# Kernel tuning notes

Hardware: AMD Instinct MI355X
Metric: run time of the kernel (lower is better)

## Reference

```python
import jax, jax.numpy as jnp
import numpy as np
from jax import lax

H = 32  # hidden size (hardcoded in the torch module)

def setup_inputs() -> dict:
    key = jax.random.key(0)
    ks = jax.random.split(key, 7)
    B, T, I = 2048, 512, 64
    s = 1.0 / np.sqrt(H)  # torch nn.LSTM default init scale
    return {
        "x": jax.random.normal(ks[0], (B, T, I), dtype=jnp.float32),
        "W_ih": jax.random.uniform(ks[1], (4 * H, I), jnp.float32, -s, s),
        "W_hh": jax.random.uniform(ks[2], (4 * H, H), jnp.float32, -s, s),
        "b_ih": jax.random.uniform(ks[3], (4 * H,), jnp.float32, -s, s),
        "b_hh": jax.random.uniform(ks[4], (4 * H,), jnp.float32, -s, s),
        "W_fc": jax.random.uniform(ks[5], (1, H), jnp.float32, -s, s),
        "b_fc": jax.random.uniform(ks[6], (1,), jnp.float32, -s, s),
    }

def _lstm_last_h(x, W_ih, W_hh, b_ih, b_hh):
    B = x.shape[0]
    # Precompute input projections for all timesteps: [B, T, 4H] -> [T, B, 4H]
    xg = jnp.einsum('bti,gi->btg', x, W_ih) + (b_ih + b_hh)
    xg = jnp.transpose(xg, (1, 0, 2))

    def step(carry, xt):
        h, c = carry
        g = xt + h @ W_hh.T  # [B, 4H]
        i = jax.nn.sigmoid(g[:, 0 * H:1 * H])
        f = jax.nn.sigmoid(g[:, 1 * H:2 * H])
        gg = jnp.tanh(g[:, 2 * H:3 * H])
        o = jax.nn.sigmoid(g[:, 3 * H:4 * H])
        c = f * c + i * gg
        h = o * jnp.tanh(c)
        return (h, c), None

    init = (jnp.zeros((B, H), x.dtype), jnp.zeros((B, H), x.dtype))
    (h, _), _ = lax.scan(step, init, xg)
    return h  # [B, H], last timestep hidden state

def reference(x, W_ih, W_hh, b_ih, b_hh, W_fc, b_fc):
    # Dropout is identity in eval mode; only the last timestep feeds fc.
    h = _lstm_last_h(x, W_ih, W_hh, b_ih, b_hh)
    return h @ W_fc.T + b_fc  # [B, 1]
```

## Files before the change

kernel.cpp:

```cpp
#include <hip/hip_runtime.h>

typedef __attribute__((ext_vector_type(8))) short short8;
typedef __attribute__((ext_vector_type(4))) float f32x4;

#define LOG2E 1.44269504088896340736f

__device__ __forceinline__ unsigned short f2bf(float f) {
    union { float f; unsigned u; } a; a.f = f;
    unsigned r = a.u + 0x7fffu + ((a.u >> 16) & 1u);
    return (unsigned short)(r >> 16);
}
__device__ __forceinline__ unsigned pk2(float x, float y) {
    return (unsigned)f2bf(x) | ((unsigned)f2bf(y) << 16);
}
__device__ __forceinline__ float sigm(float x) {
    return __builtin_amdgcn_rcpf(1.0f + __builtin_amdgcn_exp2f(-LOG2E * x));
}

__global__ __launch_bounds__(256, 2) void lstm_fused(
    const float* __restrict__ x,
    const float* __restrict__ Wih,
    const float* __restrict__ Whh,
    const float* __restrict__ bih,
    const float* __restrict__ bhh,
    const float* __restrict__ Wfc,
    const float* __restrict__ bfc,
    float* __restrict__ out)
{
    __shared__ unsigned short Wlds[128 * 80];
    __shared__ float xg_sh[4 * 16 * 132];
    __shared__ alignas(64) unsigned short hbuf[4 * 32];

    const int tid  = threadIdx.x;
    const int lane = tid & 63;
    const int wv   = tid >> 6;
    const int b    = blockIdx.x * 4 + wv;
    const int m    = lane & 15;
    const int quad = lane >> 4;
    const int cc   = lane & 31;

    {
        const float4* w4 = (const float4*)Wih;
        unsigned* wl = (unsigned*)Wlds;
        #pragma unroll
        for (int i = 0; i < 8; i++) {
            int fi = tid * 8 + i;
            int g  = fi >> 4;
            int k  = (fi & 15) << 2;
            float4 v = w4[fi];
            wl[g * 40 + (k >> 1) + 0] = pk2(v.x, v.y);
            wl[g * 40 + (k >> 1) + 1] = pk2(v.z, v.w);
        }
    }

    short8 Bh[8];
    #pragma unroll
    for (int t = 0; t < 8; t++) {
        const float4* wr = (const float4*)(Whh + (size_t)(16 * t + m) * 32 + quad * 8);
        float4 va = wr[0], vb = wr[1];
        union { short8 v; unsigned u[4]; } B;
        B.u[0] = pk2(va.x, va.y); B.u[1] = pk2(va.z, va.w);
        B.u[2] = pk2(vb.x, vb.y); B.u[3] = pk2(vb.z, vb.w);
        Bh[t] = B.v;
    }

    float biasv[8];
    #pragma unroll
    for (int n = 0; n < 8; n++) biasv[n] = bih[16 * n + m] + bhh[16 * n + m];

    const bool b4 = (lane & 16) != 0;

    __syncthreads();

    const float* xrow = x + ((size_t)b * 512 + m) * 64;
    float* xgw = xg_sh + wv * 2112;
    unsigned short* hw = hbuf + wv * 32;

    hw[cc] = 0;
    float c = 0.0f, h = 0.0f;
    const f32x4 z4 = {0.f, 0.f, 0.f, 0.f};

    float4 p0, p1, p2, p3;
    {
        const float4* xr4 = (const float4*)xrow;
        p0 = xr4[quad * 2];     p1 = xr4[quad * 2 + 1];
        p2 = xr4[8 + quad * 2]; p3 = xr4[8 + quad * 2 + 1];
    }

    for (int ch = 0; ch < 32; ++ch) {
        union { short8 v; unsigned u[4]; } A0, A1;
        A0.u[0] = pk2(p0.x, p0.y); A0.u[1] = pk2(p0.z, p0.w);
        A0.u[2] = pk2(p1.x, p1.y); A0.u[3] = pk2(p1.z, p1.w);
        A1.u[0] = pk2(p2.x, p2.y); A1.u[1] = pk2(p2.z, p2.w);
        A1.u[2] = pk2(p3.x, p3.y); A1.u[3] = pk2(p3.z, p3.w);

        {
            const int chn = (ch < 31) ? ch + 1 : 31;
            const float4* nx = (const float4*)(xrow + (size_t)chn * 1024);
            p0 = nx[quad * 2];     p1 = nx[quad * 2 + 1];
            p2 = nx[8 + quad * 2]; p3 = nx[8 + quad * 2 + 1];
        }

        #pragma unroll
        for (int n = 0; n < 8; n++) {
            const short8 B0 = *(const short8*)&Wlds[(16 * n + m) * 80 + quad * 8];
            const short8 B1 = *(const short8*)&Wlds[(16 * n + m) * 80 + 32 + quad * 8];
            f32x4 acc = {0.f, 0.f, 0.f, 0.f};
            acc = __builtin_amdgcn_mfma_f32_16x16x32_bf16(A0.v, B0, acc, 0, 0, 0);
            acc = __builtin_amdgcn_mfma_f32_16x16x32_bf16(A1.v, B1, acc, 0, 0, 0);
            const int pos = ((n & 1) << 6) + 4 * m + (n >> 1);
            #pragma unroll
            for (int r = 0; r < 4; r++)
                xgw[(quad * 4 + r) * 132 + pos] = acc[r] + biasv[n];
        }

        #pragma unroll
        for (int tt = 0; tt < 16; ++tt) {
            const short8 abf = *(const short8*)&hw[quad * 8];
            const f32x4 a0 = __builtin_amdgcn_mfma_f32_16x16x32_bf16(abf, Bh[0], z4, 0, 0, 0);
            const f32x4 a1 = __builtin_amdgcn_mfma_f32_16x16x32_bf16(abf, Bh[1], z4, 0, 0, 0);
            const f32x4 a2 = __builtin_amdgcn_mfma_f32_16x16x32_bf16(abf, Bh[2], z4, 0, 0, 0);
            const f32x4 a3 = __builtin_amdgcn_mfma_f32_16x16x32_bf16(abf, Bh[3], z4, 0, 0, 0);
            const f32x4 a4 = __builtin_amdgcn_mfma_f32_16x16x32_bf16(abf, Bh[4], z4, 0, 0, 0);
            const f32x4 a5 = __builtin_amdgcn_mfma_f32_16x16x32_bf16(abf, Bh[5], z4, 0, 0, 0);
            const f32x4 a6 = __builtin_amdgcn_mfma_f32_16x16x32_bf16(abf, Bh[6], z4, 0, 0, 0);
            const f32x4 a7 = __builtin_amdgcn_mfma_f32_16x16x32_bf16(abf, Bh[7], z4, 0, 0, 0);
            const float hi = b4 ? a1[0] : a0[0];
            const float hf = b4 ? a3[0] : a2[0];
            const float hg = b4 ? a5[0] : a4[0];
            const float ho = b4 ? a7[0] : a6[0];

            const f32x4 xg4 = *(const f32x4*)&xgw[tt * 132 + 4 * cc];
            const float gi = xg4[0] + hi;
            const float gf = xg4[1] + hf;
            const float gg = xg4[2] + hg;
            const float go = xg4[3] + ho;

            const float iv = sigm(gi);
            const float fv = sigm(gf);
            const float gv = fmaf(2.0f, sigm(2.0f * gg), -1.0f);
            const float ov = sigm(go);
            c = fmaf(fv, c, iv * gv);
            const float th = fmaf(2.0f, sigm(2.0f * c), -1.0f);
            h = ov * th;
            hw[cc] = f2bf(h);
        }
    }

    float p = (lane < 32) ? h * Wfc[cc] : 0.0f;
    #pragma unroll
    for (int msk = 16; msk >= 1; msk >>= 1) p += __shfl_xor(p, msk);
    if (lane == 0) out[b] = p + bfc[0];
}

extern "C" void kernel_launch(void* const* d_in, const int* in_sizes, int n_in,
                              void* d_out, int out_size, void* d_ws, size_t ws_size,
                              hipStream_t stream) {
    const float* x   = (const float*)d_in[0];
    const float* Wih = (const float*)d_in[1];
    const float* Whh = (const float*)d_in[2];
    const float* bih = (const float*)d_in[3];
    const float* bhh = (const float*)d_in[4];
    const float* Wfc = (const float*)d_in[5];
    const float* bfc = (const float*)d_in[6];
    float* out = (float*)d_out;
    lstm_fused<<<dim3(512), dim3(256), 0, stream>>>(x, Wih, Whh, bih, bhh, Wfc, bfc, out);
}
```

Baseline: 431.6 us.

## Process two batch rows per wavefront in the LSTM recurrence

Each wavefront now handles two batch elements instead of one. Both rows go through the same recurrent MFMA, using different A-operand rows, and the 32 lanes per half run the gate math, which had left half the lanes idle. The grid is halved to 256 blocks, LDS for the xg and h buffers doubles, and launch bounds drop to 1 block per SM. This cuts the total number of serial recurrence steps across the machine, but it lowers occupancy and adds more x-projection work per chunk.

```diff
diff --git a/kernel.cpp b/kernel.cpp
--- a/kernel.cpp
+++ b/kernel.cpp
@@ -17,7 +17,7 @@
     return __builtin_amdgcn_rcpf(1.0f + __builtin_amdgcn_exp2f(-LOG2E * x));
 }
 
-__global__ __launch_bounds__(256, 2) void lstm_fused(
+__global__ __launch_bounds__(256, 1) void lstm_fused(
     const float* __restrict__ x,
     const float* __restrict__ Wih,
     const float* __restrict__ Whh,
@@ -28,16 +28,17 @@
     float* __restrict__ out)
 {
     __shared__ unsigned short Wlds[128 * 80];
-    __shared__ float xg_sh[4 * 16 * 132];
-    __shared__ alignas(64) unsigned short hbuf[4 * 32];
+    __shared__ float xg_sh[4 * 2 * 16 * 132];
+    __shared__ alignas(64) unsigned short hbuf[4 * 64];
 
     const int tid  = threadIdx.x;
     const int lane = tid & 63;
     const int wv   = tid >> 6;
-    const int b    = blockIdx.x * 4 + wv;
+    const int b0   = blockIdx.x * 8 + wv * 2;
     const int m    = lane & 15;
     const int quad = lane >> 4;
     const int cc   = lane & 31;
+    const int rb   = lane >> 5;
 
     {
         const float4* w4 = (const float4*)Wih;
@@ -72,51 +73,67 @@
 
     __syncthreads();
 
-    const float* xrow = x + ((size_t)b * 512 + m) * 64;
-    float* xgw = xg_sh + wv * 2112;
-    unsigned short* hw = hbuf + wv * 32;
+    const float* xrow0 = x + ((size_t)b0 * 512 + m) * 64;
+    const float* xrow1 = xrow0 + 512 * 64;
+    float* xgw = xg_sh + wv * 4224;
+    unsigned short* hw = hbuf + wv * 64;
 
-    hw[cc] = 0;
+    hw[lane] = 0;
     float c = 0.0f, h = 0.0f;
     const f32x4 z4 = {0.f, 0.f, 0.f, 0.f};
 
-    float4 p0, p1, p2, p3;
+    float4 p0, p1, p2, p3, q0, q1, q2, q3;
     {
-        const float4* xr4 = (const float4*)xrow;
-        p0 = xr4[quad * 2];     p1 = xr4[quad * 2 + 1];
-        p2 = xr4[8 + quad * 2]; p3 = xr4[8 + quad * 2 + 1];
+        const float4* r0 = (const float4*)xrow0;
+        const float4* r1 = (const float4*)xrow1;
+        p0 = r0[quad * 2];     p1 = r0[quad * 2 + 1];
+        p2 = r0[8 + quad * 2]; p3 = r0[8 + quad * 2 + 1];
+        q0 = r1[quad * 2];     q1 = r1[quad * 2 + 1];
+        q2 = r1[8 + quad * 2]; q3 = r1[8 + quad * 2 + 1];
     }
 
     for (int ch = 0; ch < 32; ++ch) {
-        union { short8 v; unsigned u[4]; } A0, A1;
+        union { short8 v; unsigned u[4]; } A0, A1, C0, C1;
         A0.u[0] = pk2(p0.x, p0.y); A0.u[1] = pk2(p0.z, p0.w);
         A0.u[2] = pk2(p1.x, p1.y); A0.u[3] = pk2(p1.z, p1.w);
         A1.u[0] = pk2(p2.x, p2.y); A1.u[1] = pk2(p2.z, p2.w);
         A1.u[2] = pk2(p3.x, p3.y); A1.u[3] = pk2(p3.z, p3.w);
+        C0.u[0] = pk2(q0.x, q0.y); C0.u[1] = pk2(q0.z, q0.w);
+        C0.u[2] = pk2(q1.x, q1.y); C0.u[3] = pk2(q1.z, q1.w);
+        C1.u[0] = pk2(q2.x, q2.y); C1.u[1] = pk2(q2.z, q2.w);
+        C1.u[2] = pk2(q3.x, q3.y); C1.u[3] = pk2(q3.z, q3.w);
 
         {
             const int chn = (ch < 31) ? ch + 1 : 31;
-            const float4* nx = (const float4*)(xrow + (size_t)chn * 1024);
-            p0 = nx[quad * 2];     p1 = nx[quad * 2 + 1];
-            p2 = nx[8 + quad * 2]; p3 = nx[8 + quad * 2 + 1];
+            const float4* n0 = (const float4*)(xrow0 + (size_t)chn * 1024);
+            const float4* n1 = (const float4*)(xrow1 + (size_t)chn * 1024);
+            p0 = n0[quad * 2];     p1 = n0[quad * 2 + 1];
+            p2 = n0[8 + quad * 2]; p3 = n0[8 + quad * 2 + 1];
+            q0 = n1[quad * 2];     q1 = n1[quad * 2 + 1];
+            q2 = n1[8 + quad * 2]; q3 = n1[8 + quad * 2 + 1];
         }
 
         #pragma unroll
         for (int n = 0; n < 8; n++) {
             const short8 B0 = *(const short8*)&Wlds[(16 * n + m) * 80 + quad * 8];
             const short8 B1 = *(const short8*)&Wlds[(16 * n + m) * 80 + 32 + quad * 8];
-            f32x4 acc = {0.f, 0.f, 0.f, 0.f};
-            acc = __builtin_amdgcn_mfma_f32_16x16x32_bf16(A0.v, B0, acc, 0, 0, 0);
-            acc = __builtin_amdgcn_mfma_f32_16x16x32_bf16(A1.v, B1, acc, 0, 0, 0);
+            f32x4 ar0 = {0.f, 0.f, 0.f, 0.f};
+            ar0 = __builtin_amdgcn_mfma_f32_16x16x32_bf16(A0.v, B0, ar0, 0, 0, 0);
+            ar0 = __builtin_amdgcn_mfma_f32_16x16x32_bf16(A1.v, B1, ar0, 0, 0, 0);
+            f32x4 ar1 = {0.f, 0.f, 0.f, 0.f};
+            ar1 = __builtin_amdgcn_mfma_f32_16x16x32_bf16(C0.v, B0, ar1, 0, 0, 0);
+            ar1 = __builtin_amdgcn_mfma_f32_16x16x32_bf16(C1.v, B1, ar1, 0, 0, 0);
             const int pos = ((n & 1) << 6) + 4 * m + (n >> 1);
             #pragma unroll
-            for (int r = 0; r < 4; r++)
-                xgw[(quad * 4 + r) * 132 + pos] = acc[r] + biasv[n];
+            for (int r = 0; r < 4; r++) {
+                xgw[(quad * 4 + r) * 132 + pos]        = ar0[r] + biasv[n];
+                xgw[2112 + (quad * 4 + r) * 132 + pos] = ar1[r] + biasv[n];
+            }
         }
 
         #pragma unroll
         for (int tt = 0; tt < 16; ++tt) {
-            const short8 abf = *(const short8*)&hw[quad * 8];
+            const short8 abf = *(const short8*)&hw[((m >> 3) << 5) + quad * 8];
             const f32x4 a0 = __builtin_amdgcn_mfma_f32_16x16x32_bf16(abf, Bh[0], z4, 0, 0, 0);
             const f32x4 a1 = __builtin_amdgcn_mfma_f32_16x16x32_bf16(abf, Bh[1], z4, 0, 0, 0);
             const f32x4 a2 = __builtin_amdgcn_mfma_f32_16x16x32_bf16(abf, Bh[2], z4, 0, 0, 0);
@@ -130,7 +147,7 @@
             const float hg = b4 ? a5[0] : a4[0];
             const float ho = b4 ? a7[0] : a6[0];
 
-            const f32x4 xg4 = *(const f32x4*)&xgw[tt * 132 + 4 * cc];
+            const f32x4 xg4 = *(const f32x4*)&xgw[rb * 2112 + tt * 132 + 4 * cc];
             const float gi = xg4[0] + hi;
             const float gf = xg4[1] + hf;
             const float gg = xg4[2] + hg;
@@ -143,14 +160,14 @@
             c = fmaf(fv, c, iv * gv);
             const float th = fmaf(2.0f, sigm(2.0f * c), -1.0f);
             h = ov * th;
-            hw[cc] = f2bf(h);
+            hw[lane] = f2bf(h);
         }
     }
 
-    float p = (lane < 32) ? h * Wfc[cc] : 0.0f;
+    float p = h * Wfc[cc];
     #pragma unroll
     for (int msk = 16; msk >= 1; msk >>= 1) p += __shfl_xor(p, msk);
-    if (lane == 0) out[b] = p + bfc[0];
+    if ((lane & 31) == 0) out[b0 + rb] = p + bfc[0];
 }
 
 extern "C" void kernel_launch(void* const* d_in, const int* in_sizes, int n_in,
@@ -164,5 +181,5 @@
     const float* Wfc = (const float*)d_in[5];
     const float* bfc = (const float*)d_in[6];
     float* out = (float*)d_out;
-    lstm_fused<<<dim3(512), dim3(256), 0, stream>>>(x, Wih, Whh, bih, bhh, Wfc, bfc, out);
+    lstm_fused<<<dim3(256), dim3(256), 0, stream>>>(x, Wih, Whh, bih, bhh, Wfc, bfc, out);
 }
```

Result: faster. 419.8 us (-2.7%).
